# Kernel tuning notes

Hardware: AMD Instinct MI355X
Metric: run time of the kernel (lower is better)

The kernel has to match this reference:

```python
import jax, jax.numpy as jnp
import numpy as np
import math

D_MSA = 384
N_HEAD = 12
D_HID = 32


def setup_inputs() -> dict:
    key = jax.random.key(0)
    k1, k2, k3, k4, k5 = jax.random.split(key, 5)
    b, n, l = 2, 256, 384
    msa = jax.random.normal(k1, (b, n, l, D_MSA), dtype=jnp.float32)
    # xavier_uniform for (out, in) = (n_head*d_hidden, d_msa)
    fan_out, fan_in = N_HEAD * D_HID, D_MSA
    bound = math.sqrt(6.0 / (fan_in + fan_out))
    Wq = jax.random.uniform(k2, (fan_out, fan_in), jnp.float32, -bound, bound)
    Wk = jax.random.uniform(k3, (fan_out, fan_in), jnp.float32, -bound, bound)
    bq = jnp.zeros((fan_out,), jnp.float32)
    bk = jnp.zeros((fan_out,), jnp.float32)
    return {"msa": msa, "Wq": Wq, "bq": bq, "Wk": Wk, "bk": bk}


def reference(msa, Wq, bq, Wk, bk):
    b, n, l, _ = msa.shape
    scale = 1.0 / math.sqrt(D_HID)
    tar_seq = msa[:, 0]  # (b, l, d_msa) -- query comes from first MSA row
    q = (tar_seq @ Wq.T + bq).reshape(b, l, N_HEAD, D_HID) * scale  # (b,l,h,d)
    k = (msa @ Wk.T + bk).reshape(b, n, l, N_HEAD, D_HID)           # (b,n,l,h,d)
    # einsum('bqihd,bkihd->bkihq') with q==1 -> (b,n,l,h,1)
    attn = jnp.einsum('blhd,bnlhd->bnlh', q, k)[..., None]
    # softmax over MSA-depth axis (dim=1); dropout is identity at eval
    return jax.nn.softmax(attn, axis=1)
```

## Files before the change

### kernel.cpp

```cpp
#include <hip/hip_runtime.h>
#include <hip/hip_bf16.h>

#define D_MSA 384
#define NHEAD 12
#define DHID  32
#define BB    2
#define NN    256
#define LL    384
#define NBL   (BB * LL)
#define WFROW (NHEAD * D_MSA)

#define WF_OFF 0
#define WF_SZ  ((size_t)NBL * WFROW)
#define Q_OFF  (WF_OFF + WF_SZ)
#define Q_SZ   ((size_t)NBL * D_MSA)
#define CB_OFF (Q_OFF + Q_SZ)
#define CB_SZ  ((size_t)NBL * NHEAD)
#define LOG_OFF (CB_OFF + CB_SZ)
#define LOG_SZ ((size_t)NBL * NHEAD * NN)
#define WS_FLOATS (LOG_OFF + LOG_SZ)
#define WS_BYTES  (WS_FLOATS * 4)

__global__ __launch_bounds__(256)
void seqw_a1(const float* __restrict__ msa, const float* __restrict__ Wq,
             const float* __restrict__ bq, const float* __restrict__ bk,
             float* __restrict__ q_ws, float* __restrict__ cb_ws)
{
  __shared__ float tar[3][D_MSA];
  __shared__ float qs[3][D_MSA];
  const int t    = threadIdx.x;
  const int lane = t & 63;
  const int wv   = t >> 6;
  const int rowi = lane >> 4;
  const int seg  = lane & 15;
  const int bl0  = blockIdx.x * 3;
  const int b    = bl0 / LL, l0 = bl0 % LL;
  const float scale = 0.17677669529663687f;

  const float* base = msa + ((size_t)b * NN * LL + l0) * D_MSA;
  for (int i = t; i < 3 * D_MSA / 4; i += 256)
    ((float4*)tar)[i] = ((const float4*)base)[i];
  __syncthreads();

#pragma unroll 1
  for (int cc = 0; cc < 24; ++cc) {
    const int c = wv * 96 + cc * 4 + rowi;
    const float* wr = Wq + (size_t)c * D_MSA + seg * 4;
    float a0 = 0.f, a1 = 0.f, a2 = 0.f;
#pragma unroll
    for (int j = 0; j < 6; ++j) {
      float4 w4 = *(const float4*)(wr + 64 * j);
      float4 t0 = *(const float4*)&tar[0][64 * j + seg * 4];
      float4 t1 = *(const float4*)&tar[1][64 * j + seg * 4];
      float4 t2 = *(const float4*)&tar[2][64 * j + seg * 4];
      a0 = fmaf(w4.x, t0.x, a0); a0 = fmaf(w4.y, t0.y, a0);
      a0 = fmaf(w4.z, t0.z, a0); a0 = fmaf(w4.w, t0.w, a0);
      a1 = fmaf(w4.x, t1.x, a1); a1 = fmaf(w4.y, t1.y, a1);
      a1 = fmaf(w4.z, t1.z, a1); a1 = fmaf(w4.w, t1.w, a1);
      a2 = fmaf(w4.x, t2.x, a2); a2 = fmaf(w4.y, t2.y, a2);
      a2 = fmaf(w4.z, t2.z, a2); a2 = fmaf(w4.w, t2.w, a2);
    }
#pragma unroll
    for (int m = 8; m; m >>= 1) {
      a0 += __shfl_xor(a0, m);
      a1 += __shfl_xor(a1, m);
      a2 += __shfl_xor(a2, m);
    }
    if (seg == 0) {
      const float bqc = bq[c];
      const float q0 = scale * (a0 + bqc);
      const float q1 = scale * (a1 + bqc);
      const float q2 = scale * (a2 + bqc);
      qs[0][c] = q0; q_ws[(size_t)(bl0 + 0) * D_MSA + c] = q0;
      qs[1][c] = q1; q_ws[(size_t)(bl0 + 1) * D_MSA + c] = q1;
      qs[2][c] = q2; q_ws[(size_t)(bl0 + 2) * D_MSA + c] = q2;
    }
  }
  __syncthreads();

  if (t < 3 * NHEAD) {
    const int r = t / NHEAD, h = t % NHEAD;
    float s = 0.f;
#pragma unroll
    for (int d = 0; d < DHID; ++d)
      s = fmaf(qs[r][h * DHID + d], bk[h * DHID + d], s);
    cb_ws[(size_t)(bl0 + r) * NHEAD + h] = s;
  }
}

__global__ __launch_bounds__(256)
void seqw_a2(const float* __restrict__ Wk, const float* __restrict__ q_ws,
             float* __restrict__ wf_ws)
{
  __shared__ float qt[16][DHID];
  const int t   = threadIdx.x;
  const int h   = blockIdx.x % NHEAD;
  const int bl0 = (blockIdx.x / NHEAD) * 16;

  if (t < 128) {
    const int r = t >> 3, j = (t & 7) * 4;
    *(float4*)&qt[r][j] =
        *(const float4*)(q_ws + (size_t)(bl0 + r) * D_MSA + h * DHID + j);
  }
  __syncthreads();

#pragma unroll 1
  for (int pass = 0; pass < 2; ++pass) {
    const int c = pass * 256 + t;
    if (c < D_MSA) {
      float acc[16];
#pragma unroll
      for (int r = 0; r < 16; ++r) acc[r] = 0.f;
      const float* wkb = Wk + (size_t)(h * DHID) * D_MSA + c;
#pragma unroll 2
      for (int d = 0; d < DHID; d += 4) {
        const float w0 = wkb[(size_t)(d + 0) * D_MSA];
        const float w1 = wkb[(size_t)(d + 1) * D_MSA];
        const float w2 = wkb[(size_t)(d + 2) * D_MSA];
        const float w3 = wkb[(size_t)(d + 3) * D_MSA];
#pragma unroll
        for (int r = 0; r < 16; ++r) {
          float4 q4 = *(const float4*)&qt[r][d];
          acc[r] = fmaf(q4.x, w0, acc[r]);
          acc[r] = fmaf(q4.y, w1, acc[r]);
          acc[r] = fmaf(q4.z, w2, acc[r]);
          acc[r] = fmaf(q4.w, w3, acc[r]);
        }
      }
#pragma unroll
      for (int r = 0; r < 16; ++r)
        wf_ws[(size_t)(bl0 + r) * WFROW + h * D_MSA + c] = acc[r];
    }
  }
}

__global__ __launch_bounds__(256)
void seqw_b(const float* __restrict__ msa, const float* __restrict__ wf_ws,
            const float* __restrict__ cb_ws, float* __restrict__ log_ws)
{
  __shared__ float attn_s[NHEAD][64];
  const int t    = threadIdx.x;
  const int lane = t & 63;
  const int wv   = t >> 6;
  const int hg   = wv & 1;
  const int rq   = wv >> 1;
  const int h0   = 6 * hg;
  const int rowi = lane >> 3;
  const int seg  = lane & 7;
  const int bid  = blockIdx.x;
  const int bl   = bid >> 2;
  const int nq   = bid & 3;
  const int b    = bl / LL;
  const int l    = bl - b * LL;

  const float* wfb = wf_ws + (size_t)bl * WFROW + (size_t)h0 * D_MSA + 4 * seg;

  const size_t rstride = (size_t)LL * D_MSA;
  const float* lanebase =
      msa + ((size_t)(b * NN + nq * 64 + rq * 32 + rowi) * LL + l) * D_MSA + seg * 4;

#define LDB(buf, j)                                                             \
  {                                                                             \
    _Pragma("unroll")                                                           \
    for (int g = 0; g < 4; ++g)                                                 \
      buf[g] = *(const float4*)(lanebase + (size_t)(g * 8) * rstride + 32 * (j)); \
  }
#define CPB(buf, j)                                                             \
  {                                                                             \
    _Pragma("unroll")                                                           \
    for (int hh = 0; hh < 6; ++hh) {                                            \
      float4 w4 = *(const float4*)(wfb + (size_t)hh * D_MSA + 32 * (j));        \
      _Pragma("unroll")                                                         \
      for (int g = 0; g < 4; ++g) {                                             \
        acc[g][hh] = fmaf(buf[g].x, w4.x, acc[g][hh]);                          \
        acc[g][hh] = fmaf(buf[g].y, w4.y, acc[g][hh]);                          \
        acc[g][hh] = fmaf(buf[g].z, w4.z, acc[g][hh]);                          \
        acc[g][hh] = fmaf(buf[g].w, w4.w, acc[g][hh]);                          \
      }                                                                         \
    }                                                                           \
  }

  float acc[4][6];
#pragma unroll
  for (int g = 0; g < 4; ++g)
#pragma unroll
    for (int hh = 0; hh < 6; ++hh) acc[g][hh] = 0.f;

  float4 bufA[4], bufB[4];
  LDB(bufA, 0)
#pragma unroll 1
  for (int jj = 0; jj < 6; ++jj) {
    const int j0 = 2 * jj, j1 = 2 * jj + 1;
    LDB(bufB, j1)
    CPB(bufA, j0)
    if (jj < 5) LDB(bufA, j0 + 2)
    CPB(bufB, j1)
  }

  const float* cbb = cb_ws + (size_t)bl * NHEAD + h0;
#pragma unroll
  for (int g = 0; g < 4; ++g) {
#pragma unroll
    for (int hh = 0; hh < 6; ++hh) {
      float s = acc[g][hh];
      s += __shfl_xor(s, 4);
      s += __shfl_xor(s, 2);
      s += __shfl_xor(s, 1);
      if (seg == 0)
        attn_s[h0 + hh][rq * 32 + g * 8 + rowi] = s + cbb[hh];
    }
  }
  __syncthreads();

  for (int i = t; i < NHEAD * 64 / 4; i += 256) {
    const int h = i >> 4, r4 = i & 15;
    ((float4*)log_ws)[(size_t)bl * (NHEAD * NN / 4) + h * (NN / 4) + nq * 16 + r4] =
        ((const float4*)attn_s)[i];
  }
}

__global__ __launch_bounds__(256)
void seqw_c(const float* __restrict__ log_ws, float* __restrict__ out)
{
  __shared__ float at[NHEAD][NN];
  __shared__ float smax[NHEAD], sinv[NHEAD];
  const int t    = threadIdx.x;
  const int lane = t & 63;
  const int wv   = t >> 6;
  const int bl   = blockIdx.x;
  const int b    = bl / LL;
  const int l    = bl - b * LL;

  for (int i = t; i < NHEAD * NN / 4; i += 256)
    ((float4*)at)[i] = ((const float4*)log_ws)[(size_t)bl * (NHEAD * NN / 4) + i];
  __syncthreads();

#pragma unroll
  for (int jh = 0; jh < 3; ++jh) {
    const int h = wv * 3 + jh;
    float v0 = at[h][lane];
    float v1 = at[h][lane + 64];
    float v2 = at[h][lane + 128];
    float v3 = at[h][lane + 192];
    float mx = fmaxf(fmaxf(v0, v1), fmaxf(v2, v3));
#pragma unroll
    for (int m = 32; m; m >>= 1) mx = fmaxf(mx, __shfl_xor(mx, m));
    float s = __expf(v0 - mx) + __expf(v1 - mx) + __expf(v2 - mx) + __expf(v3 - mx);
#pragma unroll
    for (int m = 32; m; m >>= 1) s += __shfl_xor(s, m);
    if (lane == 0) { smax[h] = mx; sinv[h] = 1.0f / s; }
  }
  __syncthreads();

  {
    float o[NHEAD];
#pragma unroll
    for (int h = 0; h < NHEAD; ++h)
      o[h] = __expf(at[h][t] - smax[h]) * sinv[h];
    float* ob = out + ((size_t)(b * NN + t) * LL + l) * NHEAD;
    ((float4*)ob)[0] = make_float4(o[0], o[1], o[2],  o[3]);
    ((float4*)ob)[1] = make_float4(o[4], o[5], o[6],  o[7]);
    ((float4*)ob)[2] = make_float4(o[8], o[9], o[10], o[11]);
  }
}

struct SmemF {
  float tar[D_MSA];
  float q[D_MSA];
  float wf[NHEAD][D_MSA];
  float cb[NHEAD];
  float smax[NHEAD];
  float sinv[NHEAD];
  float attn[NHEAD][NN];
};

__global__ __launch_bounds__(512, 2)
void seqw_fused_fb(const float* __restrict__ msa, const float* __restrict__ Wq,
                   const float* __restrict__ bq, const float* __restrict__ Wk,
                   const float* __restrict__ bk, float* __restrict__ out)
{
  __shared__ SmemF sm;
  const int t    = threadIdx.x;
  const int lane = t & 63;
  const int wv   = t >> 6;
  const int rowi = lane >> 4;
  const int seg  = lane & 15;
  const int bl   = blockIdx.x;
  const int b    = bl / LL;
  const int l    = bl - b * LL;
  const float scale = 0.17677669529663687f;

  const float* targ = msa + ((size_t)(b * NN) * LL + l) * D_MSA;
  if (t < 96) ((float4*)sm.tar)[t] = ((const float4*)targ)[t];
  __syncthreads();

  {
    float2 t2[3];
#pragma unroll
    for (int p = 0; p < 3; ++p) t2[p] = *(const float2*)&sm.tar[2 * lane + 128 * p];
#pragma unroll 1
    for (int j = 0; j < 48; ++j) {
      const int r = wv * 48 + j;
      const float* wr = Wq + (size_t)r * D_MSA;
      float s = 0.f;
#pragma unroll
      for (int p = 0; p < 3; ++p) {
        float2 w2 = *(const float2*)&wr[2 * lane + 128 * p];
        s = fmaf(t2[p].x, w2.x, s);
        s = fmaf(t2[p].y, w2.y, s);
      }
#pragma unroll
      for (int m = 32; m; m >>= 1) s += __shfl_xor(s, m);
      if (lane == 0) sm.q[r] = scale * (s + bq[r]);
    }
  }
  __syncthreads();

  if (t < D_MSA) {
    const int c = t;
    float a[NHEAD];
#pragma unroll
    for (int h = 0; h < NHEAD; ++h) a[h] = 0.f;
#pragma unroll 1
    for (int d = 0; d < DHID; ++d) {
#pragma unroll
      for (int h = 0; h < NHEAD; ++h)
        a[h] = fmaf(sm.q[h * DHID + d], Wk[(size_t)(h * DHID + d) * D_MSA + c], a[h]);
    }
#pragma unroll
    for (int h = 0; h < NHEAD; ++h) sm.wf[h][c] = a[h];
  }
  if (t < NHEAD) {
    float s = 0.f;
#pragma unroll
    for (int d = 0; d < DHID; ++d) s = fmaf(sm.q[t * DHID + d], bk[t * DHID + d], s);
    sm.cb[t] = s;
  }
  __syncthreads();

  const size_t rstride = (size_t)LL * D_MSA;
  const float* lanebase =
      msa + ((size_t)(b * NN + wv * 32 + rowi) * LL + l) * D_MSA + seg * 4;

#define LDF(buf, base, j)                                                       \
  {                                                                             \
    buf[0] = *(const float4*)((base) + 64 * (j));                               \
    buf[1] = *(const float4*)((base) + 4 * rstride + 64 * (j));                 \
  }
#define CPF(buf, j)                                                             \
  {                                                                             \
    _Pragma("unroll")                                                           \
    for (int h = 0; h < NHEAD; ++h) {                                           \
      float4 w4 = *(const float4*)&sm.wf[h][64 * (j) + 4 * seg];                \
      acc[0][h] = fmaf(buf[0].x, w4.x, acc[0][h]);                              \
      acc[0][h] = fmaf(buf[0].y, w4.y, acc[0][h]);                              \
      acc[0][h] = fmaf(buf[0].z, w4.z, acc[0][h]);                              \
      acc[0][h] = fmaf(buf[0].w, w4.w, acc[0][h]);                              \
      acc[1][h] = fmaf(buf[1].x, w4.x, acc[1][h]);                              \
      acc[1][h] = fmaf(buf[1].y, w4.y, acc[1][h]);                              \
      acc[1][h] = fmaf(buf[1].z, w4.z, acc[1][h]);                              \
      acc[1][h] = fmaf(buf[1].w, w4.w, acc[1][h]);                              \
    }                                                                           \
  }

  const float* pcur = lanebase;
  float4 bufA[2], bufB[2];
  LDF(bufA, pcur, 0)
#pragma unroll 1
  for (int ch = 0; ch < 4; ++ch) {
    float acc[2][NHEAD];
#pragma unroll
    for (int g = 0; g < 2; ++g)
#pragma unroll
      for (int h = 0; h < NHEAD; ++h) acc[g][h] = 0.f;
    const float* pnext = pcur + 8 * rstride;
    LDF(bufB, pcur, 1)  CPF(bufA, 0)
    LDF(bufA, pcur, 2)  CPF(bufB, 1)
    LDF(bufB, pcur, 3)  CPF(bufA, 2)
    LDF(bufA, pcur, 4)  CPF(bufB, 3)
    LDF(bufB, pcur, 5)  CPF(bufA, 4)
    if (ch < 3) LDF(bufA, pnext, 0)
    CPF(bufB, 5)
#pragma unroll
    for (int g = 0; g < 2; ++g) {
      const int n = wv * 32 + ch * 8 + g * 4 + rowi;
#pragma unroll
      for (int h = 0; h < NHEAD; ++h) {
        float s = acc[g][h];
        s += __shfl_xor(s, 8);
        s += __shfl_xor(s, 4);
        s += __shfl_xor(s, 2);
        s += __shfl_xor(s, 1);
        if (seg == 0) sm.attn[h][n] = s + sm.cb[h];
      }
    }
    pcur = pnext;
  }
  __syncthreads();

  if (wv < 6) {
#pragma unroll
    for (int jh = 0; jh < 2; ++jh) {
      const int h = wv * 2 + jh;
      float v0 = sm.attn[h][lane];
      float v1 = sm.attn[h][lane + 64];
      float v2 = sm.attn[h][lane + 128];
      float v3 = sm.attn[h][lane + 192];
      float mx = fmaxf(fmaxf(v0, v1), fmaxf(v2, v3));
#pragma unroll
      for (int m = 32; m; m >>= 1) mx = fmaxf(mx, __shfl_xor(mx, m));
      float s = __expf(v0 - mx) + __expf(v1 - mx) + __expf(v2 - mx) + __expf(v3 - mx);
#pragma unroll
      for (int m = 32; m; m >>= 1) s += __shfl_xor(s, m);
      if (lane == 0) { sm.smax[h] = mx; sm.sinv[h] = 1.0f / s; }
    }
  }
  __syncthreads();

  if (t < NN) {
    float o[NHEAD];
#pragma unroll
    for (int h = 0; h < NHEAD; ++h)
      o[h] = __expf(sm.attn[h][t] - sm.smax[h]) * sm.sinv[h];
    float* ob = out + ((size_t)(b * NN + t) * LL + l) * NHEAD;
    ((float4*)ob)[0] = make_float4(o[0], o[1], o[2],  o[3]);
    ((float4*)ob)[1] = make_float4(o[4], o[5], o[6],  o[7]);
    ((float4*)ob)[2] = make_float4(o[8], o[9], o[10], o[11]);
  }
}

extern "C" void kernel_launch(void* const* d_in, const int* in_sizes, int n_in,
                              void* d_out, int out_size, void* d_ws, size_t ws_size,
                              hipStream_t stream) {
  const float* msa = (const float*)d_in[0];
  const float* Wq  = (const float*)d_in[1];
  const float* bq  = (const float*)d_in[2];
  const float* Wk  = (const float*)d_in[3];
  const float* bk  = (const float*)d_in[4];
  float* out = (float*)d_out;

  if (ws_size >= WS_BYTES) {
    float* ws     = (float*)d_ws;
    float* wf_ws  = ws + WF_OFF;
    float* q_ws   = ws + Q_OFF;
    float* cb_ws  = ws + CB_OFF;
    float* log_ws = ws + LOG_OFF;
    seqw_a1<<<dim3(NBL / 3), dim3(256), 0, stream>>>(msa, Wq, bq, bk, q_ws, cb_ws);
    seqw_a2<<<dim3(NHEAD * (NBL / 16)), dim3(256), 0, stream>>>(Wk, q_ws, wf_ws);
    seqw_b<<<dim3(NBL * 4), dim3(256), 0, stream>>>(msa, wf_ws, cb_ws, log_ws);
    seqw_c<<<dim3(NBL), dim3(256), 0, stream>>>(log_ws, out);
  } else {
    seqw_fused_fb<<<dim3(NBL), dim3(512), 0, stream>>>(msa, Wq, bq, Wk, bk, out);
  }
}
```

Baseline: 151.3 us.

## Split seqw_b blocks by head group and stage fused weights in LDS

Each seqw_b block now handles one group of 6 heads for 64 MSA rows, so the grid doubles and each thread keeps half as many accumulators and load buffers. The per-(b,l) fused weight rows and bias are copied into shared memory once per block rather than read from global memory by every lane. The first MSA loads are issued before that copy, and the load/compute pipeline is fully unrolled. The trade-off is that the two head-group blocks now read the same MSA rows separately, so the design depends on L2 hits to avoid doubling HBM traffic.

Result: slower. 234.5 us (+55.0%).

```diff
diff --git a/kernel.cpp b/kernel.cpp
--- a/kernel.cpp
+++ b/kernel.cpp
@@ -138,68 +138,79 @@
 void seqw_b(const float* __restrict__ msa, const float* __restrict__ wf_ws,
             const float* __restrict__ cb_ws, float* __restrict__ log_ws)
 {
-  __shared__ float attn_s[NHEAD][64];
+  __shared__ float wf_s[6][D_MSA];
+  __shared__ float cb_s[6];
+  __shared__ float attn_s[6][64];
   const int t    = threadIdx.x;
   const int lane = t & 63;
   const int wv   = t >> 6;
-  const int hg   = wv & 1;
-  const int rq   = wv >> 1;
-  const int h0   = 6 * hg;
   const int rowi = lane >> 3;
   const int seg  = lane & 7;
   const int bid  = blockIdx.x;
-  const int bl   = bid >> 2;
-  const int nq   = bid & 3;
+  const int hg   = bid & 1;
+  const int nq   = (bid >> 1) & 3;
+  const int bl   = bid >> 3;
+  const int h0   = 6 * hg;
   const int b    = bl / LL;
   const int l    = bl - b * LL;
 
-  const float* wfb = wf_ws + (size_t)bl * WFROW + (size_t)h0 * D_MSA + 4 * seg;
-
   const size_t rstride = (size_t)LL * D_MSA;
   const float* lanebase =
-      msa + ((size_t)(b * NN + nq * 64 + rq * 32 + rowi) * LL + l) * D_MSA + seg * 4;
+      msa + ((size_t)(b * NN + nq * 64 + wv * 16 + rowi) * LL + l) * D_MSA + seg * 4;
 
 #define LDB(buf, j)                                                             \
   {                                                                             \
-    _Pragma("unroll")                                                           \
-    for (int g = 0; g < 4; ++g)                                                 \
-      buf[g] = *(const float4*)(lanebase + (size_t)(g * 8) * rstride + 32 * (j)); \
+    buf[0] = *(const float4*)(lanebase + 32 * (j));                             \
+    buf[1] = *(const float4*)(lanebase + (size_t)(8) * rstride + 32 * (j));     \
   }
 #define CPB(buf, j)                                                             \
   {                                                                             \
     _Pragma("unroll")                                                           \
     for (int hh = 0; hh < 6; ++hh) {                                            \
-      float4 w4 = *(const float4*)(wfb + (size_t)hh * D_MSA + 32 * (j));        \
-      _Pragma("unroll")                                                         \
-      for (int g = 0; g < 4; ++g) {                                             \
-        acc[g][hh] = fmaf(buf[g].x, w4.x, acc[g][hh]);                          \
-        acc[g][hh] = fmaf(buf[g].y, w4.y, acc[g][hh]);                          \
-        acc[g][hh] = fmaf(buf[g].z, w4.z, acc[g][hh]);                          \
-        acc[g][hh] = fmaf(buf[g].w, w4.w, acc[g][hh]);                          \
-      }                                                                         \
+      float4 w4 = *(const float4*)&wf_s[hh][32 * (j) + 4 * seg];                \
+      acc[0][hh] = fmaf(buf[0].x, w4.x, acc[0][hh]);                            \
+      acc[0][hh] = fmaf(buf[0].y, w4.y, acc[0][hh]);                            \
+      acc[0][hh] = fmaf(buf[0].z, w4.z, acc[0][hh]);                            \
+      acc[0][hh] = fmaf(buf[0].w, w4.w, acc[0][hh]);                            \
+      acc[1][hh] = fmaf(buf[1].x, w4.x, acc[1][hh]);                            \
+      acc[1][hh] = fmaf(buf[1].y, w4.y, acc[1][hh]);                            \
+      acc[1][hh] = fmaf(buf[1].z, w4.z, acc[1][hh]);                            \
+      acc[1][hh] = fmaf(buf[1].w, w4.w, acc[1][hh]);                            \
     }                                                                           \
   }
 
-  float acc[4][6];
-#pragma unroll
-  for (int g = 0; g < 4; ++g)
+  float4 bufA[2], bufB[2];
+  LDB(bufA, 0)
+  LDB(bufB, 1)
+
+  {
+    const float4* src = (const float4*)(wf_ws + (size_t)bl * WFROW + (size_t)h0 * D_MSA);
+    for (int i = t; i < 6 * D_MSA / 4; i += 256) ((float4*)wf_s)[i] = src[i];
+    if (t < 6) cb_s[t] = cb_ws[(size_t)bl * NHEAD + h0 + t];
+  }
+  __syncthreads();
+
+  float acc[2][6];
+#pragma unroll
+  for (int g = 0; g < 2; ++g)
 #pragma unroll
     for (int hh = 0; hh < 6; ++hh) acc[g][hh] = 0.f;
 
-  float4 bufA[4], bufB[4];
-  LDB(bufA, 0)
-#pragma unroll 1
-  for (int jj = 0; jj < 6; ++jj) {
-    const int j0 = 2 * jj, j1 = 2 * jj + 1;
-    LDB(bufB, j1)
-    CPB(bufA, j0)
-    if (jj < 5) LDB(bufA, j0 + 2)
-    CPB(bufB, j1)
-  }
-
-  const float* cbb = cb_ws + (size_t)bl * NHEAD + h0;
-#pragma unroll
-  for (int g = 0; g < 4; ++g) {
+  CPB(bufA, 0)   LDB(bufA, 2)
+  CPB(bufB, 1)   LDB(bufB, 3)
+  CPB(bufA, 2)   LDB(bufA, 4)
+  CPB(bufB, 3)   LDB(bufB, 5)
+  CPB(bufA, 4)   LDB(bufA, 6)
+  CPB(bufB, 5)   LDB(bufB, 7)
+  CPB(bufA, 6)   LDB(bufA, 8)
+  CPB(bufB, 7)   LDB(bufB, 9)
+  CPB(bufA, 8)   LDB(bufA, 10)
+  CPB(bufB, 9)   LDB(bufB, 11)
+  CPB(bufA, 10)
+  CPB(bufB, 11)
+
+#pragma unroll
+  for (int g = 0; g < 2; ++g) {
 #pragma unroll
     for (int hh = 0; hh < 6; ++hh) {
       float s = acc[g][hh];
@@ -207,14 +218,14 @@
       s += __shfl_xor(s, 2);
       s += __shfl_xor(s, 1);
       if (seg == 0)
-        attn_s[h0 + hh][rq * 32 + g * 8 + rowi] = s + cbb[hh];
-    }
-  }
-  __syncthreads();
-
-  for (int i = t; i < NHEAD * 64 / 4; i += 256) {
-    const int h = i >> 4, r4 = i & 15;
-    ((float4*)log_ws)[(size_t)bl * (NHEAD * NN / 4) + h * (NN / 4) + nq * 16 + r4] =
+        attn_s[hh][wv * 16 + g * 8 + rowi] = s + cb_s[hh];
+    }
+  }
+  __syncthreads();
+
+  for (int i = t; i < 6 * 64 / 4; i += 256) {
+    const int hh = i >> 4, r4 = i & 15;
+    ((float4*)log_ws)[(size_t)bl * (NHEAD * NN / 4) + (h0 + hh) * (NN / 4) + nq * 16 + r4] =
         ((const float4*)attn_s)[i];
   }
 }
@@ -447,7 +458,7 @@
     float* log_ws = ws + LOG_OFF;
     seqw_a1<<<dim3(NBL / 3), dim3(256), 0, stream>>>(msa, Wq, bq, bk, q_ws, cb_ws);
     seqw_a2<<<dim3(NHEAD * (NBL / 16)), dim3(256), 0, stream>>>(Wk, q_ws, wf_ws);
-    seqw_b<<<dim3(NBL * 4), dim3(256), 0, stream>>>(msa, wf_ws, cb_ws, log_ws);
+    seqw_b<<<dim3(NBL * 8), dim3(256), 0, stream>>>(msa, wf_ws, cb_ws, log_ws);
     seqw_c<<<dim3(NBL), dim3(256), 0, stream>>>(log_ws, out);
   } else {
     seqw_fused_fb<<<dim3(NBL), dim3(512), 0, stream>>>(msa, Wq, bq, Wk, bk, out);
```
